# Kernel tuning notes

Measured on AMD Instinct MI355X. Metric: run time of the kernel, lower is better.

Reference implementation:

```python
import jax, jax.numpy as jnp
import numpy as np

P = 7    # output_size (7,7)
SR = 2   # sampling_ratio per bin (torchvision roi_align samples per bin)


def _roi_avg_pool(feature_map, rois):
    """Fused roi_align(output_size=PxP) + adaptive_avg_pool2d(1,1).

    Since every bin averages SR*SR equally-weighted samples and the global
    average pool then averages the P*P bins, the result equals the mean over
    all P*SR x P*SR bilinear samples -- the 7x7 grid is never materialized.
    """
    B, C, H, W = feature_map.shape
    bidx = rois[:, 0].astype(jnp.int32)                       # [N]
    # get_anns: fp32 math, stored into an fp16 tensor (replicate the rounding).
    # NOTE (faithful to source): x coords are scaled by H (shape[2]) and y by W.
    f16 = lambda v: v.astype(jnp.float16).astype(jnp.float32)
    x1 = f16((rois[:, 2] - 0.5 * rois[:, 4]) * H)
    y1 = f16((rois[:, 3] - 0.5 * rois[:, 5]) * W)
    x2 = f16((rois[:, 2] + 0.5 * rois[:, 4]) * H)
    y2 = f16((rois[:, 3] + 0.5 * rois[:, 5]) * W)

    # torchvision roi_align, spatial_scale=1, aligned=False
    roi_w = jnp.maximum(x2 - x1, 1.0)
    roi_h = jnp.maximum(y2 - y1, 1.0)
    # sample offsets: bin pw plus (ix+0.5)/SR within the bin, in units of bin size
    offs = (jnp.arange(P, dtype=jnp.float32)[:, None]
            + (jnp.arange(SR, dtype=jnp.float32)[None, :] + 0.5) / SR).reshape(-1)  # [P*SR]
    xs = x1[:, None] + offs[None, :] * (roi_w / P)[:, None]   # [N,S] along width
    ys = y1[:, None] + offs[None, :] * (roi_h / P)[:, None]   # [N,S] along height

    valid = (((ys > -1.0) & (ys < H))[:, :, None]
             & ((xs > -1.0) & (xs < W))[:, None, :])          # [N,S,S]
    yc = jnp.clip(ys, 0.0, H - 1.0)
    xc = jnp.clip(xs, 0.0, W - 1.0)
    y0 = jnp.floor(yc).astype(jnp.int32)
    x0 = jnp.floor(xc).astype(jnp.int32)
    y1i = jnp.minimum(y0 + 1, H - 1)
    x1i = jnp.minimum(x0 + 1, W - 1)
    ly = yc - y0
    lx = xc - x0
    hy = 1.0 - ly
    hx = 1.0 - lx

    feat_t = jnp.transpose(feature_map, (0, 2, 3, 1))         # [B,H,W,C]

    def gather(yy, xx):  # yy,xx: [N,S] -> [N,S,S,C]
        return feat_t[bidx[:, None, None], yy[:, :, None], xx[:, None, :]]

    w = lambda a, b: (a[:, :, None] * b[:, None, :])[..., None]
    val = (w(hy, hx) * gather(y0, x0) + w(hy, lx) * gather(y0, x1i)
           + w(ly, hx) * gather(y1i, x0) + w(ly, lx) * gather(y1i, x1i))
    val = jnp.where(valid[..., None], val, 0.0)
    return val.mean(axis=(1, 2))                              # [N,C]


def setup_inputs() -> dict:
    key = jax.random.key(0)
    k1, k2, k3, k4 = jax.random.split(key, 4)
    B, C, H, W, N = 4, 256, 128, 128, 512
    feature_map = jax.random.normal(k1, (B, C, H, W), dtype=jnp.float32)
    # sorted batch indices so the original per-batch regrouping keeps ROI order
    bidx = jnp.sort(jax.random.randint(k2, (N,), 0, B)).astype(jnp.float32)
    cls = jax.random.randint(k3, (N,), 0, 20).astype(jnp.float32)
    kc, kw = jax.random.split(k4)
    cxcy = jax.random.uniform(kc, (N, 2), minval=0.2, maxval=0.8, dtype=jnp.float32)
    wh = jax.random.uniform(kw, (N, 2), minval=0.05, maxval=0.4, dtype=jnp.float32)
    rois = jnp.concatenate([bidx[:, None], cls[:, None], cxcy, wh], axis=1)  # [N,6]
    return {"feature_map": feature_map, "rois": rois}


def reference(feature_map, rois):
    roi_feats = _roi_avg_pool(feature_map, rois)   # [N, C] (original returns len-N list of [1,C])
    gt = rois[:, 1]                                # class labels
    return roi_feats, gt
```

## Files before the change

### kernel.cpp

```cpp
#include <hip/hip_runtime.h>
#include <hip/hip_fp16.h>
#include <hip/hip_bf16.h>

#define PP 7
#define SR 2
#define HH 128
#define WW 128
#define CC 256
#define PLANE (HH * WW)
#define SLOT_BYTES 32768
#define WY_BASE (8 * SLOT_BYTES)

typedef unsigned int uint;
typedef short bf16x8 __attribute__((ext_vector_type(8)));
typedef float f32x16 __attribute__((ext_vector_type(16)));

typedef const __attribute__((address_space(1))) void g_void;
typedef __attribute__((address_space(3))) void l_void;

__device__ __forceinline__ void gload_lds16(const void* g, void* lds_base) {
  __builtin_amdgcn_global_load_lds((g_void*)g, (l_void*)lds_base, 16, 0, 0);
}

__device__ __forceinline__ uint pkbf(float a, float b) {
  __hip_bfloat16 ha = __float2bfloat16(a), hb = __float2bfloat16(b);
  return (uint)*(unsigned short*)&ha | ((uint)*(unsigned short*)&hb << 16);
}

__device__ __forceinline__ int lb_img(const float* rois, int N, float v) {
  int lo = 0, hi = N;
  while (lo < hi) {
    const int mid = (lo + hi) >> 1;
    if (rois[mid * 6] < v) lo = mid + 1; else hi = mid;
  }
  return lo;
}

__global__ __launch_bounds__(64) void roi_meta_kernel(
    const float* __restrict__ rois, unsigned char* wsb,
    float* __restrict__ out, int N, int B) {
  const int roi = blockIdx.x;
  const int lane = threadIdx.x;

  __shared__ float WXs[WW], WYs[HH];
  WXs[lane] = 0.f; WXs[lane + 64] = 0.f;
  WYs[lane] = 0.f; WYs[lane + 64] = 0.f;

  int lbv = 0;
  if (lane <= B) lbv = lb_img(rois, N, (float)lane);
  __syncthreads();

  const float bf = rois[roi * 6 + 0];
  const float cx = rois[roi * 6 + 2];
  const float cy = rois[roi * 6 + 3];
  const float w_ = rois[roi * 6 + 4];
  const float h_ = rois[roi * 6 + 5];

  const float x1 = __half2float(__float2half(
      __fmul_rn(__fsub_rn(cx, __fmul_rn(0.5f, w_)), 128.0f)));
  const float y1 = __half2float(__float2half(
      __fmul_rn(__fsub_rn(cy, __fmul_rn(0.5f, h_)), 128.0f)));
  const float x2 = __half2float(__float2half(
      __fmul_rn(__fadd_rn(cx, __fmul_rn(0.5f, w_)), 128.0f)));
  const float y2 = __half2float(__float2half(
      __fmul_rn(__fadd_rn(cy, __fmul_rn(0.5f, h_)), 128.0f)));

  const float sx = fmaxf(__fsub_rn(x2, x1), 1.0f) / 7.0f;
  const float sy = fmaxf(__fsub_rn(y2, y1), 1.0f) / 7.0f;

  if (lane < 2 * PP * SR) {
    const int isX = lane >= PP * SR;
    const int i = lane - isX * PP * SR;
    const float off = (float)(i >> 1) + ((float)(i & 1) + 0.5f) * 0.5f;
    const float pos = __fadd_rn(isX ? x1 : y1, __fmul_rn(off, isX ? sx : sy));
    if (pos > -1.0f && pos < 128.0f) {
      const float pc = fminf(fmaxf(pos, 0.0f), 127.0f);
      const int p0 = (int)floorf(pc);
      const int p1 = min(p0 + 1, 127);
      const float l = pc - (float)p0;
      float* Warr = isX ? WXs : WYs;
      atomicAdd(&Warr[p0], 1.0f - l);
      atomicAdd(&Warr[p1], l);
    }
  }
  __syncthreads();

  const int img = (int)bf;
  const int myStart = __shfl(lbv, img, 64);
  int tb = 0;
  for (int i = 0; i < img; ++i)
    tb += (__shfl(lbv, i + 1, 64) - __shfl(lbv, i, 64) + 127) >> 7;
  const int rl = roi - myStart;
  const int slot = tb + (rl >> 7);
  const int col = rl & 127;
  const int ni = col >> 5, c31 = col & 31;

  const int sw = ((((lane >> 2) ^ (col & 7)) << 4) | ((lane & 3) << 2));
  *(uint*)(wsb + (size_t)slot * SLOT_BYTES + col * 256 + sw) =
      pkbf(WXs[2 * lane], WXs[2 * lane + 1]);

  unsigned char* wyb = wsb + WY_BASE + (size_t)slot * SLOT_BYTES;
  #pragma unroll
  for (int h = 0; h < 2; ++h) {
    const int y = lane + 64 * h;
    const int mtile = y >> 5, y5 = y & 31;
    const int ahalf = (y5 >> 2) & 1;
    const int j = (y5 & 3) | ((y5 >> 3) << 2);
    const int ln = c31 | (ahalf << 5);
    __hip_bfloat16 hv = __float2bfloat16(WYs[y]);
    *(unsigned short*)(wyb + ((((mtile << 2) | ni) << 6 | ln) << 5) + (j << 1)) =
        *(unsigned short*)&hv;
  }

  if (lane == 0) out[(size_t)N * CC + roi] = rois[roi * 6 + 1];
}

__global__ __launch_bounds__(256, 2) void roi_gemm_kernel(
    const float* __restrict__ fm, const float* __restrict__ rois,
    const unsigned char* __restrict__ wsb, float* __restrict__ out,
    int N, int B) {
  const int bid = blockIdx.x;
  const int ch = bid & (CC - 1);
  const int img = bid >> 8;
  const int t = threadIdx.x, wave = t >> 6, lane = t & 63;

  int lbv = 0;
  if (lane <= B) lbv = lb_img(rois, N, (float)lane);
  const int istart = __shfl(lbv, img, 64);
  const int cnt = __shfl(lbv, img + 1, 64) - istart;
  if (cnt == 0) return;
  int tbase = 0;
  for (int i = 0; i < img; ++i)
    tbase += (__shfl(lbv, i + 1, 64) - __shfl(lbv, i, 64) + 127) >> 7;
  const int tcnt = (cnt + 127) >> 7;

  __shared__ unsigned char A[32768];
  __shared__ unsigned char BXl[32768];
  __shared__ float partial[4][128];

  auto stage_bx = [&](int ti) {
    const unsigned char* BXg = wsb + (size_t)(tbase + ti) * SLOT_BYTES;
    #pragma unroll
    for (int k2 = 0; k2 < 8; ++k2)
      gload_lds16(BXg + k2 * 4096 + wave * 1024 + (lane << 4),
                  BXl + k2 * 4096 + wave * 1024);
  };

  stage_bx(0);

  const float* pb = fm + ((size_t)img * CC + ch) * PLANE;
  float4 u[16];
  #pragma unroll
  for (int k = 0; k < 8; ++k) {
    const int cid = k * 256 + t;
    u[2 * k]     = *(const float4*)(pb + (size_t)cid * 8);
    u[2 * k + 1] = *(const float4*)(pb + (size_t)cid * 8 + 4);
  }
  __builtin_amdgcn_sched_barrier(0);
  #pragma unroll
  for (int k = 0; k < 8; ++k) {
    const int cid = k * 256 + t;
    const int row = cid >> 4, x8 = cid & 15;
    const int boff = (row << 8) | ((x8 ^ (row & 7)) << 4);
    uint4 P;
    P.x = pkbf(u[2 * k].x, u[2 * k].y); P.y = pkbf(u[2 * k].z, u[2 * k].w);
    P.z = pkbf(u[2 * k + 1].x, u[2 * k + 1].y); P.w = pkbf(u[2 * k + 1].z, u[2 * k + 1].w);
    *(uint4*)(A + boff) = P;
  }
  asm volatile("s_waitcnt vmcnt(0)" ::: "memory");
  __syncthreads();

  const int m0 = wave * 32;
  const int arow = m0 + (lane & 31);
  const int ar7 = arow & 7;
  const unsigned char* Arow = A + (arow << 8);
  const int ahalf = lane >> 5;
  const int r7 = lane & 7;

  for (int ti = 0; ti < tcnt; ++ti) {
    if (ti > 0) {
      stage_bx(ti);
      asm volatile("s_waitcnt vmcnt(0)" ::: "memory");
      __syncthreads();
    }
    const unsigned char* BYc = wsb + WY_BASE + (size_t)(tbase + ti) * SLOT_BYTES;

    f32x16 ac0 = {}, ac1 = {}, ac2 = {}, ac3 = {};

    auto ldA = [&](int ks) -> bf16x8 {
      const int idx = (ahalf + 2 * ks) ^ ar7;
      return *(const bf16x8*)(Arow + (idx << 4));
    };
    auto ldB = [&](int ks, int ni) -> bf16x8 {
      const int c = (2 * ks + ahalf) ^ r7;
      return *(const bf16x8*)(BXl + (((lane & 31) + 32 * ni) << 8) + (c << 4));
    };

    bf16x8 a = ldA(0);
    bf16x8 b0 = ldB(0, 0), b1 = ldB(0, 1), b2 = ldB(0, 2), b3 = ldB(0, 3);
    #pragma unroll
    for (int ks = 0; ks < 8; ++ks) {
      bf16x8 an{}, bn0{}, bn1{}, bn2{}, bn3{};
      if (ks < 7) {
        an = ldA(ks + 1);
        bn0 = ldB(ks + 1, 0); bn1 = ldB(ks + 1, 1);
        bn2 = ldB(ks + 1, 2); bn3 = ldB(ks + 1, 3);
      }
      ac0 = __builtin_amdgcn_mfma_f32_32x32x16_bf16(a, b0, ac0, 0, 0, 0);
      ac1 = __builtin_amdgcn_mfma_f32_32x32x16_bf16(a, b1, ac1, 0, 0, 0);
      ac2 = __builtin_amdgcn_mfma_f32_32x32x16_bf16(a, b2, ac2, 0, 0, 0);
      ac3 = __builtin_amdgcn_mfma_f32_32x32x16_bf16(a, b3, ac3, 0, 0, 0);
      a = an; b0 = bn0; b1 = bn1; b2 = bn2; b3 = bn3;
    }

    #pragma unroll
    for (int ni = 0; ni < 4; ++ni) {
      const f32x16 acc = ni == 0 ? ac0 : ni == 1 ? ac1 : ni == 2 ? ac2 : ac3;
      const uint* wp = (const uint*)(
          BYc + ((((wave << 2) | ni) << 6 | lane) << 5));
      const uint4 wlo = *(const uint4*)wp;
      const uint4 whi = *(const uint4*)(wp + 4);
      float p = 0.f;
      p = fmaf(__uint_as_float(wlo.x << 16),         acc[0], p);
      p = fmaf(__uint_as_float(wlo.x & 0xffff0000u), acc[1], p);
      p = fmaf(__uint_as_float(wlo.y << 16),         acc[2], p);
      p = fmaf(__uint_as_float(wlo.y & 0xffff0000u), acc[3], p);
      p = fmaf(__uint_as_float(wlo.z << 16),         acc[4], p);
      p = fmaf(__uint_as_float(wlo.z & 0xffff0000u), acc[5], p);
      p = fmaf(__uint_as_float(wlo.w << 16),         acc[6], p);
      p = fmaf(__uint_as_float(wlo.w & 0xffff0000u), acc[7], p);
      p = fmaf(__uint_as_float(whi.x << 16),         acc[8], p);
      p = fmaf(__uint_as_float(whi.x & 0xffff0000u), acc[9], p);
      p = fmaf(__uint_as_float(whi.y << 16),         acc[10], p);
      p = fmaf(__uint_as_float(whi.y & 0xffff0000u), acc[11], p);
      p = fmaf(__uint_as_float(whi.z << 16),         acc[12], p);
      p = fmaf(__uint_as_float(whi.z & 0xffff0000u), acc[13], p);
      p = fmaf(__uint_as_float(whi.w << 16),         acc[14], p);
      p = fmaf(__uint_as_float(whi.w & 0xffff0000u), acc[15], p);
      p += __shfl_xor(p, 32, 64);
      if (lane < 32) partial[wave][ni * 32 + lane] = p;
    }
    __syncthreads();
    if (t < 128) {
      const int rl = ti * 128 + t;
      if (rl < cnt) {
        const float s = partial[0][t] + partial[1][t] + partial[2][t] + partial[3][t];
        out[(size_t)(istart + rl) * CC + ch] = s * (1.0f / 196.0f);
      }
    }
    __syncthreads();
  }
}

extern "C" void kernel_launch(void* const* d_in, const int* in_sizes, int n_in,
                              void* d_out, int out_size, void* d_ws, size_t ws_size,
                              hipStream_t stream) {
  const float* fm   = (const float*)d_in[0];
  const float* rois = (const float*)d_in[1];
  float* out = (float*)d_out;
  unsigned char* wsb = (unsigned char*)d_ws;
  const int N = in_sizes[1] / 6;
  const int B = in_sizes[0] / (CC * PLANE);
  roi_meta_kernel<<<N, 64, 0, stream>>>(rois, wsb, out, N, B);
  roi_gemm_kernel<<<B * CC, 256, 0, stream>>>(fm, rois, wsb, out, N, B);
}
```

Baseline: 33.89 us.

## Process two channels per block with prefetched second feature plane

Each block now handles two channels of one image, issuing global loads for both 64KB feature planes up front so the second plane's load overlaps the first plane's conversion and MFMA work. The BX staging tile is reused across both channels when the image has a single ROI tile, which avoids reloading it. The grid is halved to 512 blocks, and each thread holds 32 float4 registers for the two planes. This raises register pressure and may hurt occupancy or per-CU parallelism.

```diff
diff --git a/kernel.cpp b/kernel.cpp
--- a/kernel.cpp
+++ b/kernel.cpp
@@ -115,13 +115,34 @@
   if (lane == 0) out[(size_t)N * CC + roi] = rois[roi * 6 + 1];
 }
 
+#define ISSUE_PLANE(u, cc) do { \
+  const float* pb_ = pimg + (size_t)(c0 + (cc)) * PLANE; \
+  _Pragma("unroll") \
+  for (int k_ = 0; k_ < 8; ++k_) { \
+    const int cid_ = k_ * 256 + t; \
+    u[2*k_]   = *(const float4*)(pb_ + (size_t)cid_ * 8); \
+    u[2*k_+1] = *(const float4*)(pb_ + (size_t)cid_ * 8 + 4); \
+  } } while (0)
+
+#define CONVERT_PLANE(u) do { \
+  _Pragma("unroll") \
+  for (int k_ = 0; k_ < 8; ++k_) { \
+    const int cid_ = k_ * 256 + t; \
+    const int row_ = cid_ >> 4, x8_ = cid_ & 15; \
+    const int boff_ = (row_ << 8) | ((x8_ ^ (row_ & 7)) << 4); \
+    uint4 P_; \
+    P_.x = pkbf(u[2*k_].x, u[2*k_].y);     P_.y = pkbf(u[2*k_].z, u[2*k_].w); \
+    P_.z = pkbf(u[2*k_+1].x, u[2*k_+1].y); P_.w = pkbf(u[2*k_+1].z, u[2*k_+1].w); \
+    *(uint4*)(A + boff_) = P_; \
+  } } while (0)
+
 __global__ __launch_bounds__(256, 2) void roi_gemm_kernel(
     const float* __restrict__ fm, const float* __restrict__ rois,
     const unsigned char* __restrict__ wsb, float* __restrict__ out,
     int N, int B) {
   const int bid = blockIdx.x;
-  const int ch = bid & (CC - 1);
-  const int img = bid >> 8;
+  const int img = bid >> 7;
+  const int c0 = (bid & 127) * 2;
   const int t = threadIdx.x, wave = t >> 6, lane = t & 63;
 
   int lbv = 0;
@@ -146,30 +167,7 @@
                   BXl + k2 * 4096 + wave * 1024);
   };
 
-  stage_bx(0);
-
-  const float* pb = fm + ((size_t)img * CC + ch) * PLANE;
-  float4 u[16];
-  #pragma unroll
-  for (int k = 0; k < 8; ++k) {
-    const int cid = k * 256 + t;
-    u[2 * k]     = *(const float4*)(pb + (size_t)cid * 8);
-    u[2 * k + 1] = *(const float4*)(pb + (size_t)cid * 8 + 4);
-  }
-  __builtin_amdgcn_sched_barrier(0);
-  #pragma unroll
-  for (int k = 0; k < 8; ++k) {
-    const int cid = k * 256 + t;
-    const int row = cid >> 4, x8 = cid & 15;
-    const int boff = (row << 8) | ((x8 ^ (row & 7)) << 4);
-    uint4 P;
-    P.x = pkbf(u[2 * k].x, u[2 * k].y); P.y = pkbf(u[2 * k].z, u[2 * k].w);
-    P.z = pkbf(u[2 * k + 1].x, u[2 * k + 1].y); P.w = pkbf(u[2 * k + 1].z, u[2 * k + 1].w);
-    *(uint4*)(A + boff) = P;
-  }
-  asm volatile("s_waitcnt vmcnt(0)" ::: "memory");
-  __syncthreads();
-
+  const float* pimg = fm + (size_t)img * CC * PLANE;
   const int m0 = wave * 32;
   const int arow = m0 + (lane & 31);
   const int ar7 = arow & 7;
@@ -177,78 +175,100 @@
   const int ahalf = lane >> 5;
   const int r7 = lane & 7;
 
-  for (int ti = 0; ti < tcnt; ++ti) {
-    if (ti > 0) {
-      stage_bx(ti);
-      asm volatile("s_waitcnt vmcnt(0)" ::: "memory");
+  float4 uC[16], uN[16];
+
+  stage_bx(0);
+  int curtile = 0;
+  ISSUE_PLANE(uC, 0);
+  ISSUE_PLANE(uN, 1);
+  __builtin_amdgcn_sched_barrier(0);
+
+  #pragma unroll
+  for (int c = 0; c < 2; ++c) {
+    if (c == 0) asm volatile("s_waitcnt vmcnt(16)" ::: "memory");
+    else        asm volatile("s_waitcnt vmcnt(0)"  ::: "memory");
+    __builtin_amdgcn_sched_barrier(0);
+    __syncthreads();
+    if (c == 0) CONVERT_PLANE(uC); else CONVERT_PLANE(uN);
+    __syncthreads();
+
+    for (int ti = 0; ti < tcnt; ++ti) {
+      if (curtile != ti) {
+        __syncthreads();
+        stage_bx(ti);
+        asm volatile("s_waitcnt vmcnt(0)" ::: "memory");
+        __syncthreads();
+        curtile = ti;
+      }
+      const unsigned char* BYc =
+          wsb + WY_BASE + (size_t)(tbase + ti) * SLOT_BYTES;
+
+      f32x16 ac0 = {}, ac1 = {}, ac2 = {}, ac3 = {};
+
+      auto ldA = [&](int ks) -> bf16x8 {
+        const int idx = (ahalf + 2 * ks) ^ ar7;
+        return *(const bf16x8*)(Arow + (idx << 4));
+      };
+      auto ldB = [&](int ks, int ni) -> bf16x8 {
+        const int csw = (2 * ks + ahalf) ^ r7;
+        return *(const bf16x8*)(BXl + (((lane & 31) + 32 * ni) << 8) + (csw << 4));
+      };
+
+      bf16x8 a = ldA(0);
+      bf16x8 b0 = ldB(0, 0), b1 = ldB(0, 1), b2 = ldB(0, 2), b3 = ldB(0, 3);
+      #pragma unroll
+      for (int ks = 0; ks < 8; ++ks) {
+        bf16x8 an{}, bn0{}, bn1{}, bn2{}, bn3{};
+        if (ks < 7) {
+          an = ldA(ks + 1);
+          bn0 = ldB(ks + 1, 0); bn1 = ldB(ks + 1, 1);
+          bn2 = ldB(ks + 1, 2); bn3 = ldB(ks + 1, 3);
+        }
+        ac0 = __builtin_amdgcn_mfma_f32_32x32x16_bf16(a, b0, ac0, 0, 0, 0);
+        ac1 = __builtin_amdgcn_mfma_f32_32x32x16_bf16(a, b1, ac1, 0, 0, 0);
+        ac2 = __builtin_amdgcn_mfma_f32_32x32x16_bf16(a, b2, ac2, 0, 0, 0);
+        ac3 = __builtin_amdgcn_mfma_f32_32x32x16_bf16(a, b3, ac3, 0, 0, 0);
+        a = an; b0 = bn0; b1 = bn1; b2 = bn2; b3 = bn3;
+      }
+
+      #pragma unroll
+      for (int ni = 0; ni < 4; ++ni) {
+        const f32x16 acc = ni == 0 ? ac0 : ni == 1 ? ac1 : ni == 2 ? ac2 : ac3;
+        const uint* wp = (const uint*)(
+            BYc + ((((wave << 2) | ni) << 6 | lane) << 5));
+        const uint4 wlo = *(const uint4*)wp;
+        const uint4 whi = *(const uint4*)(wp + 4);
+        float p = 0.f;
+        p = fmaf(__uint_as_float(wlo.x << 16),         acc[0], p);
+        p = fmaf(__uint_as_float(wlo.x & 0xffff0000u), acc[1], p);
+        p = fmaf(__uint_as_float(wlo.y << 16),         acc[2], p);
+        p = fmaf(__uint_as_float(wlo.y & 0xffff0000u), acc[3], p);
+        p = fmaf(__uint_as_float(wlo.z << 16),         acc[4], p);
+        p = fmaf(__uint_as_float(wlo.z & 0xffff0000u), acc[5], p);
+        p = fmaf(__uint_as_float(wlo.w << 16),         acc[6], p);
+        p = fmaf(__uint_as_float(wlo.w & 0xffff0000u), acc[7], p);
+        p = fmaf(__uint_as_float(whi.x << 16),         acc[8], p);
+        p = fmaf(__uint_as_float(whi.x & 0xffff0000u), acc[9], p);
+        p = fmaf(__uint_as_float(whi.y << 16),         acc[10], p);
+        p = fmaf(__uint_as_float(whi.y & 0xffff0000u), acc[11], p);
+        p = fmaf(__uint_as_float(whi.z << 16),         acc[12], p);
+        p = fmaf(__uint_as_float(whi.z & 0xffff0000u), acc[13], p);
+        p = fmaf(__uint_as_float(whi.w << 16),         acc[14], p);
+        p = fmaf(__uint_as_float(whi.w & 0xffff0000u), acc[15], p);
+        p += __shfl_xor(p, 32, 64);
+        if (lane < 32) partial[wave][ni * 32 + lane] = p;
+      }
+      __syncthreads();
+      if (t < 128) {
+        const int rl = ti * 128 + t;
+        if (rl < cnt) {
+          const float s =
+              partial[0][t] + partial[1][t] + partial[2][t] + partial[3][t];
+          out[(size_t)(istart + rl) * CC + (c0 + c)] = s * (1.0f / 196.0f);
+        }
+      }
       __syncthreads();
     }
-    const unsigned char* BYc = wsb + WY_BASE + (size_t)(tbase + ti) * SLOT_BYTES;
-
-    f32x16 ac0 = {}, ac1 = {}, ac2 = {}, ac3 = {};
-
-    auto ldA = [&](int ks) -> bf16x8 {
-      const int idx = (ahalf + 2 * ks) ^ ar7;
-      return *(const bf16x8*)(Arow + (idx << 4));
-    };
-    auto ldB = [&](int ks, int ni) -> bf16x8 {
-      const int c = (2 * ks + ahalf) ^ r7;
-      return *(const bf16x8*)(BXl + (((lane & 31) + 32 * ni) << 8) + (c << 4));
-    };
-
-    bf16x8 a = ldA(0);
-    bf16x8 b0 = ldB(0, 0), b1 = ldB(0, 1), b2 = ldB(0, 2), b3 = ldB(0, 3);
-    #pragma unroll
-    for (int ks = 0; ks < 8; ++ks) {
-      bf16x8 an{}, bn0{}, bn1{}, bn2{}, bn3{};
-      if (ks < 7) {
-        an = ldA(ks + 1);
-        bn0 = ldB(ks + 1, 0); bn1 = ldB(ks + 1, 1);
-        bn2 = ldB(ks + 1, 2); bn3 = ldB(ks + 1, 3);
-      }
-      ac0 = __builtin_amdgcn_mfma_f32_32x32x16_bf16(a, b0, ac0, 0, 0, 0);
-      ac1 = __builtin_amdgcn_mfma_f32_32x32x16_bf16(a, b1, ac1, 0, 0, 0);
-      ac2 = __builtin_amdgcn_mfma_f32_32x32x16_bf16(a, b2, ac2, 0, 0, 0);
-      ac3 = __builtin_amdgcn_mfma_f32_32x32x16_bf16(a, b3, ac3, 0, 0, 0);
-      a = an; b0 = bn0; b1 = bn1; b2 = bn2; b3 = bn3;
-    }
-
-    #pragma unroll
-    for (int ni = 0; ni < 4; ++ni) {
-      const f32x16 acc = ni == 0 ? ac0 : ni == 1 ? ac1 : ni == 2 ? ac2 : ac3;
-      const uint* wp = (const uint*)(
-          BYc + ((((wave << 2) | ni) << 6 | lane) << 5));
-      const uint4 wlo = *(const uint4*)wp;
-      const uint4 whi = *(const uint4*)(wp + 4);
-      float p = 0.f;
-      p = fmaf(__uint_as_float(wlo.x << 16),         acc[0], p);
-      p = fmaf(__uint_as_float(wlo.x & 0xffff0000u), acc[1], p);
-      p = fmaf(__uint_as_float(wlo.y << 16),         acc[2], p);
-      p = fmaf(__uint_as_float(wlo.y & 0xffff0000u), acc[3], p);
-      p = fmaf(__uint_as_float(wlo.z << 16),         acc[4], p);
-      p = fmaf(__uint_as_float(wlo.z & 0xffff0000u), acc[5], p);
-      p = fmaf(__uint_as_float(wlo.w << 16),         acc[6], p);
-      p = fmaf(__uint_as_float(wlo.w & 0xffff0000u), acc[7], p);
-      p = fmaf(__uint_as_float(whi.x << 16),         acc[8], p);
-      p = fmaf(__uint_as_float(whi.x & 0xffff0000u), acc[9], p);
-      p = fmaf(__uint_as_float(whi.y << 16),         acc[10], p);
-      p = fmaf(__uint_as_float(whi.y & 0xffff0000u), acc[11], p);
-      p = fmaf(__uint_as_float(whi.z << 16),         acc[12], p);
-      p = fmaf(__uint_as_float(whi.z & 0xffff0000u), acc[13], p);
-      p = fmaf(__uint_as_float(whi.w << 16),         acc[14], p);
-      p = fmaf(__uint_as_float(whi.w & 0xffff0000u), acc[15], p);
-      p += __shfl_xor(p, 32, 64);
-      if (lane < 32) partial[wave][ni * 32 + lane] = p;
-    }
-    __syncthreads();
-    if (t < 128) {
-      const int rl = ti * 128 + t;
-      if (rl < cnt) {
-        const float s = partial[0][t] + partial[1][t] + partial[2][t] + partial[3][t];
-        out[(size_t)(istart + rl) * CC + ch] = s * (1.0f / 196.0f);
-      }
-    }
-    __syncthreads();
   }
 }
 
@@ -262,5 +282,5 @@
   const int N = in_sizes[1] / 6;
   const int B = in_sizes[0] / (CC * PLANE);
   roi_meta_kernel<<<N, 64, 0, stream>>>(rois, wsb, out, N, B);
-  roi_gemm_kernel<<<B * CC, 256, 0, stream>>>(fm, rois, wsb, out, N, B);
-}
+  roi_gemm_kernel<<<B * 128, 256, 0, stream>>>(fm, rois, wsb, out, N, B);
+}
```

Result: slower. 34.79 us (+2.7%).
